# Kernel optimization log

Measured on AMD Instinct MI355X. Metric: run time of the kernel, lower is better.

The kernel has to match this reference:

```python
import jax, jax.numpy as jnp
import numpy as np

B, N, G, K, ENC = 8, 8192, 512, 32, 512
EPS = 1e-5


def setup_inputs() -> dict:
    key = jax.random.key(0)
    ks = jax.random.split(key, 8)
    def rn(k, shape, scale):
        return jax.random.normal(k, shape, dtype=jnp.float32) * scale
    return {
        "xyz": jax.random.normal(ks[0], (B, N, 3), dtype=jnp.float32),
        "color": jax.random.uniform(ks[1], (B, N, 3), dtype=jnp.float32),
        # Encoder.first_conv: Conv1d(6,128,1) -> LN(128) -> ReLU -> Conv1d(128,256,1)
        "w1": rn(ks[2], (128, 6), 0.4),   "b1": jnp.zeros((128,), jnp.float32),
        "g1": jnp.ones((128,), jnp.float32), "be1": jnp.zeros((128,), jnp.float32),
        "w2": rn(ks[3], (256, 128), 0.08), "b2": jnp.zeros((256,), jnp.float32),
        # Encoder.second_conv: Conv1d(512,512,1) -> LN(512) -> ReLU -> Conv1d(512,ENC,1)
        "w3": rn(ks[4], (512, 512), 0.04), "b3": jnp.zeros((512,), jnp.float32),
        "g2": jnp.ones((512,), jnp.float32), "be2": jnp.zeros((512,), jnp.float32),
        "w4": rn(ks[5], (ENC, 512), 0.04), "b4": jnp.zeros((ENC,), jnp.float32),
    }


def _fps_idx(xyz, num_samples):
    # Iterative farthest-point sampling, deterministic start at index 0 (pytorch3d default).
    b, n, _ = xyz.shape
    def body(carry, _):
        min_d, last = carry                                   # [B,N], [B]
        lp = jnp.take_along_axis(xyz, last[:, None, None], axis=1)  # [B,1,3]
        d = jnp.sum((xyz - lp) ** 2, axis=-1)                 # [B,N]
        min_d = jnp.minimum(min_d, d)
        nxt = jnp.argmax(min_d, axis=1).astype(jnp.int32)
        return (min_d, nxt), nxt
    init = (jnp.full((b, n), jnp.inf, dtype=xyz.dtype), jnp.zeros((b,), jnp.int32))
    _, rest = jax.lax.scan(body, init, None, length=num_samples - 1)
    return jnp.concatenate([jnp.zeros((1, b), jnp.int32), rest], axis=0).T  # [B,G]


def _layer_norm(x, g, b):
    mu = jnp.mean(x, axis=-1, keepdims=True)
    var = jnp.mean((x - mu) ** 2, axis=-1, keepdims=True)
    return (x - mu) * jax.lax.rsqrt(var + EPS) * g + b


def reference(xyz, color, w1, b1, g1, be1, w2, b2, w3, b3, g2, be2, w4, b4):
    # ---- Group: FPS centers + full pairwise sqdist + KNN top-k + gathers ----
    fidx = _fps_idx(xyz, G)                                   # [B,G]
    center = jax.vmap(lambda p, i: p[i])(xyz, fidx)           # [B,G,3]
    # square_distance(center, xyz) -> [B,G,N]
    d = (-2.0 * jnp.einsum('bgc,bnc->bgn', center, xyz)
         + jnp.sum(center ** 2, axis=-1)[:, :, None]
         + jnp.sum(xyz ** 2, axis=-1)[:, None, :])
    _, knn = jax.lax.top_k(-d, K)                             # [B,G,K] smallest distances
    gather = jax.vmap(lambda p, i: p[i])
    nbr_xyz = gather(xyz, knn.reshape(B, -1)).reshape(B, G, K, 3)
    nbr_col = gather(color, knn.reshape(B, -1)).reshape(B, G, K, 3)
    feats = jnp.concatenate([nbr_xyz - center[:, :, None, :], nbr_col], axis=-1)  # [B,G,K,6]
    # ---- Encoder: 1x1 convs == per-point linears (layer_norm variant) ----
    x = feats.reshape(B * G, K, 6)
    h = jnp.einsum('pkc,dc->pkd', x, w1) + b1                 # [BG,K,128]
    h = jax.nn.relu(_layer_norm(h, g1, be1))
    h = jnp.einsum('pkc,dc->pkd', h, w2) + b2                 # [BG,K,256]
    hg = jnp.max(h, axis=1, keepdims=True)                    # [BG,1,256] global max-pool
    h = jnp.concatenate([jnp.broadcast_to(hg, h.shape), h], axis=-1)  # [BG,K,512]
    h = jnp.einsum('pkc,dc->pkd', h, w3) + b3                 # [BG,K,512]
    h = jax.nn.relu(_layer_norm(h, g2, be2))
    h = jnp.einsum('pkc,dc->pkd', h, w4) + b4                 # [BG,K,ENC]
    return jnp.max(h, axis=1).reshape(B, G, ENC)
```

## Files before the change

### kernel.cpp

```cpp
#include <hip/hip_runtime.h>
#include <hip/hip_bf16.h>
#include <stdint.h>

constexpr int Bn = 8;
constexpr int Np = 8192;
constexpr int Gc = 512;
constexpr int Kn = 32;
constexpr int Mrows = Bn * Gc * Kn;
constexpr float LNEPS = 1e-5f;
constexpr int CNTS = 32;

using f32x2  = __attribute__((ext_vector_type(2))) float;
using f32x4  = __attribute__((ext_vector_type(4))) float;
using bf16x8 = __attribute__((ext_vector_type(8))) __bf16;

#define DEVINL __device__ __forceinline__

DEVINL unsigned wave_red_max_u32(unsigned x) {
    int v = (int)x, t;
    t = __builtin_amdgcn_update_dpp(0, v, 0x111, 0xf, 0xf, false); v = ((unsigned)v > (unsigned)t) ? v : t;
    t = __builtin_amdgcn_update_dpp(0, v, 0x112, 0xf, 0xf, false); v = ((unsigned)v > (unsigned)t) ? v : t;
    t = __builtin_amdgcn_update_dpp(0, v, 0x114, 0xf, 0xf, false); v = ((unsigned)v > (unsigned)t) ? v : t;
    t = __builtin_amdgcn_update_dpp(0, v, 0x118, 0xf, 0xf, false); v = ((unsigned)v > (unsigned)t) ? v : t;
    t = __builtin_amdgcn_update_dpp(0, v, 0x142, 0xa, 0xf, false); v = ((unsigned)v > (unsigned)t) ? v : t;
    t = __builtin_amdgcn_update_dpp(0, v, 0x143, 0xc, 0xf, false); v = ((unsigned)v > (unsigned)t) ? v : t;
    return (unsigned)__builtin_amdgcn_readlane(v, 63);
}
DEVINL unsigned wave_red_min_u32(unsigned x) {
    int v = (int)x, t;
    t = __builtin_amdgcn_update_dpp(-1, v, 0x111, 0xf, 0xf, false); v = ((unsigned)v < (unsigned)t) ? v : t;
    t = __builtin_amdgcn_update_dpp(-1, v, 0x112, 0xf, 0xf, false); v = ((unsigned)v < (unsigned)t) ? v : t;
    t = __builtin_amdgcn_update_dpp(-1, v, 0x114, 0xf, 0xf, false); v = ((unsigned)v < (unsigned)t) ? v : t;
    t = __builtin_amdgcn_update_dpp(-1, v, 0x118, 0xf, 0xf, false); v = ((unsigned)v < (unsigned)t) ? v : t;
    t = __builtin_amdgcn_update_dpp(-1, v, 0x142, 0xa, 0xf, false); v = ((unsigned)v < (unsigned)t) ? v : t;
    t = __builtin_amdgcn_update_dpp(-1, v, 0x143, 0xc, 0xf, false); v = ((unsigned)v < (unsigned)t) ? v : t;
    return (unsigned)__builtin_amdgcn_readlane(v, 63);
}
DEVINL unsigned long long wave_red_min_u64(unsigned long long x) {
    unsigned lo = (unsigned)x, hi = (unsigned)(x >> 32);
#define RSTEP(ctl, rm) { \
    unsigned tlo = (unsigned)__builtin_amdgcn_update_dpp(-1, (int)lo, ctl, rm, 0xf, false); \
    unsigned thi = (unsigned)__builtin_amdgcn_update_dpp(-1, (int)hi, ctl, rm, 0xf, false); \
    unsigned long long o = ((unsigned long long)thi << 32) | tlo; \
    unsigned long long c = ((unsigned long long)hi << 32) | lo; \
    if (o < c) { lo = tlo; hi = thi; } }
    RSTEP(0x111, 0xf) RSTEP(0x112, 0xf) RSTEP(0x114, 0xf) RSTEP(0x118, 0xf)
    RSTEP(0x142, 0xa) RSTEP(0x143, 0xc)
#undef RSTEP
    unsigned flo = (unsigned)__builtin_amdgcn_readlane((int)lo, 63);
    unsigned fhi = (unsigned)__builtin_amdgcn_readlane((int)hi, 63);
    return ((unsigned long long)fhi << 32) | flo;
}
DEVINL unsigned fkey(float f) {
    unsigned b = __float_as_uint(f);
    return b ^ (unsigned)(((int)b >> 31) | (int)0x80000000);
}

__global__ __launch_bounds__(512) void fps_knn_h1_kernel(
    const float* __restrict__ xyz, const float* __restrict__ color,
    const float* __restrict__ w1, const float* __restrict__ b1,
    const float* __restrict__ g1, const float* __restrict__ be1,
    __hip_bfloat16* __restrict__ h1b,
    unsigned* __restrict__ cnt, unsigned* __restrict__ cidx)
{
    alignas(16) __shared__ char shraw[131104];
    const int t = threadIdx.x;

    if (blockIdx.x < 8) {
        const int b = blockIdx.x;
        f32x4* pts = (f32x4*)shraw;
        unsigned long long* sred = (unsigned long long*)(shraw + 131072);
        const float* P = xyz + (size_t)b * Np * 3;
        f32x2 X[8], Y[8], Z[8], MD[8];
#pragma unroll
        for (int i = 0; i < 8; ++i) {
            int p0 = (2 * i) * 512 + t;
            int p1 = p0 + 512;
            float x0 = P[p0 * 3 + 0], y0 = P[p0 * 3 + 1], z0 = P[p0 * 3 + 2];
            float x1 = P[p1 * 3 + 0], y1 = P[p1 * 3 + 1], z1 = P[p1 * 3 + 2];
            X[i] = f32x2{x0, x1}; Y[i] = f32x2{y0, y1}; Z[i] = f32x2{z0, z1};
            pts[p0] = f32x4{x0, y0, z0, 0.f};
            pts[p1] = f32x4{x1, y1, z1, 0.f};
            MD[i] = f32x2{__builtin_inff(), __builtin_inff()};
        }
        if (t < 3) sred[t] = 0ull;
        if (t == 0) {
            __hip_atomic_store(&cidx[b * Gc + 0], 0u, __ATOMIC_RELAXED, __HIP_MEMORY_SCOPE_AGENT);
            __hip_atomic_store(&cnt[b * CNTS], 1u, __ATOMIC_RELEASE, __HIP_MEMORY_SCOPE_AGENT);
        }
        __syncthreads();
        int last = 0;
        for (int g = 1; g < Gc; ++g) {
            const f32x4 c4 = pts[last];
            const f32x2 cx = {c4.x, c4.x}, cy = {c4.y, c4.y}, cz = {c4.z, c4.z};
            f32x2 bv2 = {0.f, 0.f};
#pragma unroll
            for (int i = 0; i < 8; ++i) {
                f32x2 dx = X[i] - cx;
                f32x2 dy = Y[i] - cy;
                f32x2 dz = Z[i] - cz;
                f32x2 d  = (dx * dx + dy * dy) + dz * dz;
                f32x2 m  = MD[i];
                m.x = fminf(m.x, d.x); m.y = fminf(m.y, d.y);
                MD[i] = m;
                bv2.x = fmaxf(bv2.x, m.x); bv2.y = fmaxf(bv2.y, m.y);
            }
            const float bv = fmaxf(bv2.x, bv2.y);
            const unsigned wmax = wave_red_max_u32(__float_as_uint(bv));
            unsigned idx = 0xffffffffu;
#pragma unroll
            for (int i = 7; i >= 0; --i) {
                if (__float_as_uint(MD[i].y) == wmax) idx = (unsigned)((2 * i + 1) * 512 + t);
                if (__float_as_uint(MD[i].x) == wmax) idx = (unsigned)((2 * i) * 512 + t);
            }
            const unsigned widx = wave_red_min_u32(idx);
            if ((t & 63) == 0) {
                unsigned long long pack =
                    ((unsigned long long)wmax << 32) | (unsigned long long)(~widx);
                atomicMax(&sred[g % 3], pack);
            }
            if (t == 1) sred[(g + 1) % 3] = 0ull;
            __syncthreads();
            const unsigned long long w = sred[g % 3];
            const int wi = (int)(~(unsigned)w);
            if (t == 0) {
                __hip_atomic_store(&cidx[b * Gc + g], (unsigned)wi, __ATOMIC_RELAXED, __HIP_MEMORY_SCOPE_AGENT);
                if ((g & 7) == 7)
                    __hip_atomic_store(&cnt[b * CNTS], (unsigned)(g + 1), __ATOMIC_RELEASE, __HIP_MEMORY_SCOPE_AGENT);
            }
            last = wi;
        }
        return;
    }

    const int cid  = blockIdx.x - 8;
    const int cb   = cid & 7;
    const int cj   = cid >> 3;
    const int wave = t >> 6;
    const int sub  = wave & 3;
    const int gsel = wave >> 2;
    const int lane = t & 63;
    unsigned long long* wl = (unsigned long long*)shraw;
    float* fs = (float*)(shraw + 2048);
    const float* P = xyz + (size_t)cb * Np * 3;
    const float* C = color + (size_t)cb * Np * 3;
    const int pbase = sub * 2048 + lane;

    for (int p = cj; p < 256; p += 31) {
        const int g = 2 * p + gsel;
        if (t == 0) {
            while ((int)__hip_atomic_load(&cnt[cb * CNTS], __ATOMIC_ACQUIRE, __HIP_MEMORY_SCOPE_AGENT) < 2 * p + 2)
                __builtin_amdgcn_s_sleep(8);
        }
        __syncthreads();
        const unsigned wic = __hip_atomic_load(&cidx[cb * Gc + g], __ATOMIC_RELAXED, __HIP_MEMORY_SCOPE_AGENT);
        const float cx = P[wic * 3 + 0], cy = P[wic * 3 + 1], cz = P[wic * 3 + 2];
        const float cc = __fadd_rn(__fadd_rn(__fmul_rn(cx, cx), __fmul_rn(cy, cy)), __fmul_rn(cz, cz));
        float dr[32];
#pragma unroll
        for (int i = 0; i < 32; ++i) {
            int pp = pbase + i * 64;
            float px = P[pp * 3 + 0], py = P[pp * 3 + 1], pz = P[pp * 3 + 2];
            float dot = __fadd_rn(__fadd_rn(__fmul_rn(cx, px), __fmul_rn(cy, py)), __fmul_rn(cz, pz));
            float q   = __fadd_rn(__fadd_rn(__fmul_rn(px, px), __fmul_rn(py, py)), __fmul_rn(pz, pz));
            dr[i] = __fadd_rn(__fadd_rn(__fmul_rn(-2.0f, dot), cc), q);
        }
        unsigned excl = 0;
        for (int k = 0; k < Kn; ++k) {
            float bd = __builtin_inff();
            int   bs = 0;
#pragma unroll
            for (int i = 0; i < 32; ++i) {
                float d = ((excl >> i) & 1u) ? __builtin_inff() : dr[i];
                if (d < bd) { bd = d; bs = i; }
            }
            unsigned gidx = (unsigned)(pbase + bs * 64);
            unsigned long long win = wave_red_min_u64(
                ((unsigned long long)fkey(bd) << 32) | (unsigned long long)gidx);
            if (lane == 0) wl[gsel * 128 + sub * 32 + k] = win;
            unsigned widx = (unsigned)win;
            if ((widx & 63) == (unsigned)lane) excl |= 1u << ((widx >> 6) & 31);
        }
        __syncthreads();
        {
            const int tt = t & 255, half = t >> 8;
            if (tt < 128) {
                const unsigned long long my = wl[half * 128 + tt];
                int rank = 0;
                for (int j = 0; j < 128; ++j) rank += (wl[half * 128 + j] < my) ? 1 : 0;
                if (rank < Kn) {
                    unsigned gi = (unsigned)my;
                    float px = P[gi * 3 + 0], py = P[gi * 3 + 1], pz = P[gi * 3 + 2];
                    float* F = fs + (half * 32 + rank) * 6;
                    F[0] = px - cx; F[1] = py - cy; F[2] = pz - cz;
                    F[3] = C[gi * 3 + 0]; F[4] = C[gi * 3 + 1]; F[5] = C[gi * 3 + 2];
                }
            }
        }
        __syncthreads();
#pragma unroll
        for (int rr = 0; rr < 8; ++rr) {
            const int r  = wave * 8 + rr;
            const int gg = r >> 5, k = r & 31;
            const float* F = fs + (gg * 32 + k) * 6;
            float fr[6];
#pragma unroll
            for (int i = 0; i < 6; ++i) fr[i] = F[i];
            const int c0 = lane * 2;
            float a0 = b1[c0], a1 = b1[c0 + 1];
#pragma unroll
            for (int i = 0; i < 6; ++i) {
                a0 = fmaf(w1[c0 * 6 + i], fr[i], a0);
                a1 = fmaf(w1[(c0 + 1) * 6 + i], fr[i], a1);
            }
            float s = a0 + a1;
#pragma unroll
            for (int m = 1; m < 64; m <<= 1) s += __shfl_xor(s, m, 64);
            float mu = s * (1.f / 128.f);
            float d0 = a0 - mu, d1 = a1 - mu;
            float q = d0 * d0 + d1 * d1;
#pragma unroll
            for (int m = 1; m < 64; m <<= 1) q += __shfl_xor(q, m, 64);
            float iv = rsqrtf(q * (1.f / 128.f) + LNEPS);
            float y0 = fmaxf(0.f, d0 * iv * g1[c0] + be1[c0]);
            float y1 = fmaxf(0.f, d1 * iv * g1[c0 + 1] + be1[c0 + 1]);
            __hip_bfloat16* dst = h1b + ((size_t)(cb * Gc + 2 * p + gg) * 32 + k) * 128 + c0;
            dst[0] = __float2bfloat16(y0);
            dst[1] = __float2bfloat16(y1);
        }
        __syncthreads();
    }
}

__global__ void cast_w_kernel(const float* __restrict__ w2, const float* __restrict__ w3,
                              const float* __restrict__ w4,
                              __hip_bfloat16* __restrict__ o2, __hip_bfloat16* __restrict__ o3,
                              __hip_bfloat16* __restrict__ o4)
{
    int i = blockIdx.x * 256 + threadIdx.x;
    if (i < 256 * 128) o2[i] = __float2bfloat16(w2[i]);
    o3[i] = __float2bfloat16(w3[i]);
    o4[i] = __float2bfloat16(w4[i]);
}

template <int BN, int BK, int EPI>
__global__ __launch_bounds__(512, 2) void gemm_kernel(
    const __hip_bfloat16* A, int lda,
    const __hip_bfloat16* __restrict__ Bw, int ldb, int nkt,
    const float* __restrict__ bias,
    const float* __restrict__ gamma, const float* __restrict__ beta,
    __hip_bfloat16* outB, int ocol0,
    float* __restrict__ outF)
{
    constexpr int BM = 128;
    constexpr int WN = BN / 4;
    constexpr int NI = WN / 16;
    constexpr int MI = 4;
    constexpr int RB = BK * 2;
    constexpr int SWM = BK / 8 - 1;
    constexpr int A_ELE = BM * BK;
    constexpr int B_ELE = BN * BK;
    constexpr int BUF = A_ELE + B_ELE;
    constexpr int ACH = A_ELE * 2 / 16 / 512;
    constexpr int BCH = B_ELE * 2 / 16 / 512;
    __shared__ __hip_bfloat16 smem[2 * BUF];

    const int tid  = threadIdx.x;
    const int wid  = tid >> 6, lane = tid & 63;
    const int wm   = wid >> 2, wn = wid & 3;
    const int lrow = lane & 15, lq = lane >> 4;
    const int m0   = blockIdx.x * BM;

    f32x4 acc[MI][NI] = {};

    auto stage = [&](int buf, int k0) {
        const char* Ab = (const char*)A + ((size_t)m0 * lda + k0) * 2;
        const char* Bb = (const char*)Bw + (size_t)k0 * 2;
        char* sA = (char*)(smem + (size_t)buf * BUF);
        char* sB = sA + A_ELE * 2;
#pragma unroll
        for (int i = 0; i < ACH; ++i) {
            int chunk = i * 512 + tid;
            int Pp = chunk * 16;
            int row = Pp / RB;
            int kb = (Pp % RB) ^ ((row & SWM) << 4);
            const void* g = Ab + (size_t)row * (lda * 2) + kb;
            void* l = sA + (i * 512 + wid * 64) * 16;
            __builtin_amdgcn_global_load_lds((const __attribute__((address_space(1))) void*)g,
                                             (__attribute__((address_space(3))) void*)l, 16, 0, 0);
        }
#pragma unroll
        for (int i = 0; i < BCH; ++i) {
            int chunk = i * 512 + tid;
            int Pp = chunk * 16;
            int n = Pp / RB;
            int kb = (Pp % RB) ^ ((n & SWM) << 4);
            const void* g = Bb + (size_t)n * (ldb * 2) + kb;
            void* l = sB + (i * 512 + wid * 64) * 16;
            __builtin_amdgcn_global_load_lds((const __attribute__((address_space(1))) void*)g,
                                             (__attribute__((address_space(3))) void*)l, 16, 0, 0);
        }
    };

    auto compute = [&](int buf) {
        const char* sA = (const char*)(smem + (size_t)buf * BUF);
        const char* sB = sA + A_ELE * 2;
#pragma unroll
        for (int kk = 0; kk < BK / 32; ++kk) {
            bf16x8 af[MI], bfv[NI];
#pragma unroll
            for (int mi = 0; mi < MI; ++mi) {
                int row = wm * 64 + mi * 16 + lrow;
                int off = row * RB + ((kk * 64 + lq * 16) ^ ((row & SWM) << 4));
                af[mi] = *(const bf16x8*)(sA + off);
            }
#pragma unroll
            for (int ni = 0; ni < NI; ++ni) {
                int n = wn * WN + ni * 16 + lrow;
                int off = n * RB + ((kk * 64 + lq * 16) ^ ((n & SWM) << 4));
                bfv[ni] = *(const bf16x8*)(sB + off);
            }
#pragma unroll
            for (int mi = 0; mi < MI; ++mi)
#pragma unroll
                for (int ni = 0; ni < NI; ++ni)
                    acc[mi][ni] = __builtin_amdgcn_mfma_f32_16x16x32_bf16(af[mi], bfv[ni], acc[mi][ni], 0, 0, 0);
        }
    };

    stage(0, 0);
    __syncthreads();
    int cur = 0;
    for (int kt = 0; kt < nkt; ++kt) {
        if (kt + 1 < nkt) stage(cur ^ 1, (kt + 1) * BK);
        compute(cur);
        __syncthreads();
        cur ^= 1;
    }

    float bv[NI] = {};
    if constexpr (EPI != 6) {
#pragma unroll
        for (int ni = 0; ni < NI; ++ni) bv[ni] = bias[wn * WN + ni * 16 + lrow];
    }

    if constexpr (EPI == 5) {
#pragma unroll
        for (int mi = 0; mi < MI; ++mi)
#pragma unroll
            for (int ni = 0; ni < NI; ++ni) {
                int col = ocol0 + wn * WN + ni * 16 + lrow;
#pragma unroll
                for (int j = 0; j < 4; ++j) {
                    int row = wm * 64 + mi * 16 + lq * 4 + j;
                    outB[(size_t)(m0 + row) * 512 + col] = __float2bfloat16(acc[mi][ni][j] + bv[ni]);
                }
            }
        __hip_bfloat16* hgc = (__hip_bfloat16*)outF;
#pragma unroll
        for (int mi2 = 0; mi2 < 2; ++mi2) {
#pragma unroll
            for (int ni = 0; ni < NI; ++ni) {
                float m = -__builtin_inff();
#pragma unroll
                for (int mh = 0; mh < 2; ++mh) {
                    int mi = mi2 * 2 + mh;
#pragma unroll
                    for (int j = 0; j < 4; ++j) m = fmaxf(m, acc[mi][ni][j] + bv[ni]);
                }
                m = fmaxf(m, __shfl_xor(m, 16, 64));
                m = fmaxf(m, __shfl_xor(m, 32, 64));
                if (lq == 0) {
                    int grow = (m0 >> 5) + wm * 2 + mi2;
                    hgc[(size_t)grow * 256 + wn * WN + ni * 16 + lrow] = __float2bfloat16(m);
                }
            }
        }
    } else if constexpr (EPI == 4) {
#pragma unroll
        for (int mi = 0; mi < MI; ++mi)
#pragma unroll
            for (int ni = 0; ni < NI; ++ni) {
                int col = wn * WN + ni * 16 + lrow;
#pragma unroll
                for (int j = 0; j < 4; ++j) {
                    int row = wm * 64 + mi * 16 + lq * 4 + j;
                    outF[(size_t)(m0 + row) * 512 + col] = acc[mi][ni][j] + bv[ni];
                }
            }
    } else if constexpr (EPI == 6) {
        float gv[NI], bev[NI];
#pragma unroll
        for (int ni = 0; ni < NI; ++ni) {
            int col = wn * WN + ni * 16 + lrow;
            gv[ni] = gamma[col]; bev[ni] = beta[col];
        }
        {
            const float* P1 = outF;
#pragma unroll
            for (int mi = 0; mi < MI; ++mi) {
                int grow = (m0 >> 5) + wm * 2 + (mi >> 1);
#pragma unroll
                for (int ni = 0; ni < NI; ++ni) {
                    float ad = P1[(size_t)grow * 512 + (wn * WN + ni * 16 + lrow)];
#pragma unroll
                    for (int j = 0; j < 4; ++j) acc[mi][ni][j] += ad;
                }
            }
        }

        float* rs  = (float*)smem;
        float* rq  = rs + BM * 4;
        float* rmu = rq + BM * 4;
        float* riv = rmu + BM;
#pragma unroll
        for (int mi = 0; mi < MI; ++mi) {
#pragma unroll
            for (int j = 0; j < 4; ++j) {
                float s = 0.f, q = 0.f;
#pragma unroll
                for (int ni = 0; ni < NI; ++ni) { float v = acc[mi][ni][j]; s += v; q += v * v; }
#pragma unroll
                for (int m = 1; m < 16; m <<= 1) { s += __shfl_xor(s, m, 64); q += __shfl_xor(q, m, 64); }
                if (lrow == 0) {
                    int row = wm * 64 + mi * 16 + lq * 4 + j;
                    rs[row * 4 + wn] = s;
                    rq[row * 4 + wn] = q;
                }
            }
        }
        __syncthreads();
        if (tid < BM) {
            float S = rs[tid * 4 + 0] + rs[tid * 4 + 1] + rs[tid * 4 + 2] + rs[tid * 4 + 3];
            float Q = rq[tid * 4 + 0] + rq[tid * 4 + 1] + rq[tid * 4 + 2] + rq[tid * 4 + 3];
            float mu = S * (1.f / BN);
            float var = Q * (1.f / BN) - mu * mu;
            rmu[tid] = mu;
            riv[tid] = rsqrtf(var + LNEPS);
        }
        __syncthreads();
#pragma unroll
        for (int mi = 0; mi < MI; ++mi)
#pragma unroll
            for (int j = 0; j < 4; ++j) {
                int row = wm * 64 + mi * 16 + lq * 4 + j;
                float mu = rmu[row], iv = riv[row];
#pragma unroll
                for (int ni = 0; ni < NI; ++ni) {
                    float v = (acc[mi][ni][j] - mu) * iv * gv[ni] + bev[ni];
                    v = fmaxf(v, 0.f);
                    outB[(size_t)(m0 + row) * 512 + (wn * WN + ni * 16 + lrow)] = __float2bfloat16(v);
                }
            }
    } else {
#pragma unroll
        for (int grp = 0; grp < 2; ++grp) {
            float mx[NI];
#pragma unroll
            for (int ni = 0; ni < NI; ++ni) {
                float m = -__builtin_inff();
#pragma unroll
                for (int mh = 0; mh < 2; ++mh) {
                    int mi = grp * 2 + mh;
#pragma unroll
                    for (int j = 0; j < 4; ++j) m = fmaxf(m, acc[mi][ni][j] + bv[ni]);
                }
                mx[ni] = m;
            }
#pragma unroll
            for (int ni = 0; ni < NI; ++ni) {
                mx[ni] = fmaxf(mx[ni], __shfl_xor(mx[ni], 16, 64));
                mx[ni] = fmaxf(mx[ni], __shfl_xor(mx[ni], 32, 64));
            }
            if (lq == 0) {
                int grow = (m0 >> 5) + wm * 2 + grp;
#pragma unroll
                for (int ni = 0; ni < NI; ++ni)
                    outF[(size_t)grow * 512 + wn * WN + ni * 16 + lrow] = mx[ni];
            }
        }
    }
}

extern "C" void kernel_launch(void* const* d_in, const int* in_sizes, int n_in,
                              void* d_out, int out_size, void* d_ws, size_t ws_size,
                              hipStream_t stream)
{
    const float* xyz   = (const float*)d_in[0];
    const float* color = (const float*)d_in[1];
    const float* w1  = (const float*)d_in[2];
    const float* b1  = (const float*)d_in[3];
    const float* g1  = (const float*)d_in[4];
    const float* be1 = (const float*)d_in[5];
    const float* w2  = (const float*)d_in[6];
    const float* b2  = (const float*)d_in[7];
    const float* w3  = (const float*)d_in[8];
    const float* b3  = (const float*)d_in[9];
    const float* g2  = (const float*)d_in[10];
    const float* be2 = (const float*)d_in[11];
    const float* w4  = (const float*)d_in[12];
    const float* b4  = (const float*)d_in[13];
    float* out = (float*)d_out;

    char* ws = (char*)d_ws;
    size_t off = 0;
    auto alloc = [&](size_t bytes) -> void* {
        void* p = ws + off;
        off += (bytes + 255) & ~(size_t)255;
        return p;
    };
    unsigned* cnt       = (unsigned*)alloc((size_t)Bn * CNTS * 4);
    unsigned* cidx      = (unsigned*)alloc((size_t)Bn * Gc * 4);
    __hip_bfloat16* w2b = (__hip_bfloat16*)alloc((size_t)256 * 128 * 2);
    __hip_bfloat16* w3b = (__hip_bfloat16*)alloc((size_t)512 * 512 * 2);
    __hip_bfloat16* w4b = (__hip_bfloat16*)alloc((size_t)512 * 512 * 2);
    __hip_bfloat16* hgc = (__hip_bfloat16*)alloc((size_t)Bn * Gc * 256 * 2);
    __hip_bfloat16* h1b = (__hip_bfloat16*)alloc((size_t)Mrows * 128 * 2);
    __hip_bfloat16* x3  = (__hip_bfloat16*)alloc((size_t)Mrows * 512 * 2);
    float* P1 = (float*)h1b;
    (void)ws_size; (void)in_sizes; (void)n_in; (void)out_size;

    hipMemsetAsync(cnt, 0, (size_t)Bn * CNTS * 4, stream);
    fps_knn_h1_kernel<<<256, 512, 0, stream>>>(xyz, color, w1, b1, g1, be1, h1b, cnt, cidx);
    cast_w_kernel<<<1024, 256, 0, stream>>>(w2, w3, w4, w2b, w3b, w4b);
    gemm_kernel<256, 32, 5><<<Mrows / 128, 512, 0, stream>>>(h1b, 128, w2b, 128, 4,  b2, nullptr, nullptr, x3, 256, (float*)hgc);
    gemm_kernel<512, 32, 4><<<Bn * Gc / 128, 512, 0, stream>>>(hgc, 256, w3b, 512, 8, b3, nullptr, nullptr, nullptr, 0, P1);
    gemm_kernel<512, 32, 6><<<Mrows / 128, 512, 0, stream>>>(x3 + 256, 512, w3b + 256, 512, 8, nullptr, g2, be2, x3, 0, P1);
    gemm_kernel<512, 32, 2><<<Mrows / 128, 512, 0, stream>>>(x3, 512, w4b, 512, 16, b4, nullptr, nullptr, nullptr, 0, out);
}
```

Baseline: 653.3 us.

## Fuse whole encoder MLP into FPS/KNN consumer blocks with LDS-resident activations

Removes the four separate GEMM launches and global intermediates (h1, x3, hg, P1). Each consumer block now runs conv2, the global-feature matvec, conv3 with LayerNorm and conv4 with max-pool on its 64 rows, keeping activations in swizzled LDS. Weights are read straight from global or L2 without LDS staging. This trades large, well-tiled GEMMs for small 64-row MFMA tiles on only 248 blocks that overlap with FPS, so the encoder can now be hidden behind the serial FPS critical path. The risk is that the compute per block becomes the bottleneck.

Measured after the change: 1.621 ms. 2.48x slower.

```diff
diff --git a/kernel.cpp b/kernel.cpp
--- a/kernel.cpp
+++ b/kernel.cpp
@@ -6,7 +6,6 @@
 constexpr int Np = 8192;
 constexpr int Gc = 512;
 constexpr int Kn = 32;
-constexpr int Mrows = Bn * Gc * Kn;
 constexpr float LNEPS = 1e-5f;
 constexpr int CNTS = 32;
 
@@ -56,11 +55,28 @@
     return b ^ (unsigned)(((int)b >> 31) | (int)0x80000000);
 }
 
-__global__ __launch_bounds__(512) void fps_knn_h1_kernel(
+constexpr int WLOFF = 0;
+constexpr int FSOFF = 2048;
+constexpr int HGOFF = 3584;
+constexpr int P1OFF = 5632;
+constexpr int RSOFF = 9728;
+constexpr int RQOFF = 11776;
+constexpr int MUOFF = 13824;
+constexpr int IVOFF = 14080;
+constexpr int H1OFF = 14336;
+constexpr int H2OFF = 30720;
+constexpr int H3OFF = 63488;
+
+__global__ __launch_bounds__(512) void fused_net_kernel(
     const float* __restrict__ xyz, const float* __restrict__ color,
     const float* __restrict__ w1, const float* __restrict__ b1,
     const float* __restrict__ g1, const float* __restrict__ be1,
-    __hip_bfloat16* __restrict__ h1b,
+    const __hip_bfloat16* __restrict__ w2b, const __hip_bfloat16* __restrict__ w3b,
+    const __hip_bfloat16* __restrict__ w4b,
+    const float* __restrict__ b2, const float* __restrict__ b3,
+    const float* __restrict__ g2, const float* __restrict__ be2,
+    const float* __restrict__ b4,
+    float* __restrict__ out,
     unsigned* __restrict__ cnt, unsigned* __restrict__ cidx)
 {
     alignas(16) __shared__ char shraw[131104];
@@ -136,12 +152,19 @@
     const int cid  = blockIdx.x - 8;
     const int cb   = cid & 7;
     const int cj   = cid >> 3;
-    const int wave = t >> 6;
-    const int sub  = wave & 3;
-    const int gsel = wave >> 2;
+    const int wid  = t >> 6;
+    const int sub  = wid & 3;
+    const int gsel = wid >> 2;
     const int lane = t & 63;
-    unsigned long long* wl = (unsigned long long*)shraw;
-    float* fs = (float*)(shraw + 2048);
+    const int lrow = lane & 15, lq = lane >> 4;
+    unsigned long long* wl = (unsigned long long*)(shraw + WLOFF);
+    float* fs  = (float*)(shraw + FSOFF);
+    float* hgs = (float*)(shraw + HGOFF);
+    float* P1s = (float*)(shraw + P1OFF);
+    float* rs64 = (float*)(shraw + RSOFF);
+    float* rq64 = (float*)(shraw + RQOFF);
+    float* rmu = (float*)(shraw + MUOFF);
+    float* riv = (float*)(shraw + IVOFF);
     const float* P = xyz + (size_t)cb * Np * 3;
     const float* C = color + (size_t)cb * Np * 3;
     const int pbase = sub * 2048 + lane;
@@ -200,9 +223,8 @@
         __syncthreads();
 #pragma unroll
         for (int rr = 0; rr < 8; ++rr) {
-            const int r  = wave * 8 + rr;
-            const int gg = r >> 5, k = r & 31;
-            const float* F = fs + (gg * 32 + k) * 6;
+            const int r = wid * 8 + rr;
+            const float* F = fs + r * 6;
             float fr[6];
 #pragma unroll
             for (int i = 0; i < 6; ++i) fr[i] = F[i];
@@ -224,9 +246,196 @@
             float iv = rsqrtf(q * (1.f / 128.f) + LNEPS);
             float y0 = fmaxf(0.f, d0 * iv * g1[c0] + be1[c0]);
             float y1 = fmaxf(0.f, d1 * iv * g1[c0 + 1] + be1[c0 + 1]);
-            __hip_bfloat16* dst = h1b + ((size_t)(cb * Gc + 2 * p + gg) * 32 + k) * 128 + c0;
-            dst[0] = __float2bfloat16(y0);
-            dst[1] = __float2bfloat16(y1);
+            __hip_bfloat16 h0 = __float2bfloat16(y0), h1v = __float2bfloat16(y1);
+            unsigned pack = (unsigned)*(unsigned short*)&h0 | ((unsigned)*(unsigned short*)&h1v << 16);
+            *(unsigned*)(shraw + H1OFF + r * 256 + ((c0 * 2) ^ ((r & 15) << 4))) = pack;
+        }
+        __syncthreads();
+        {
+            const int n0 = wid * 32;
+            f32x4 a2[4][2] = {};
+#pragma unroll
+            for (int ks = 0; ks < 4; ++ks) {
+                bf16x8 af[4], bf2[2];
+#pragma unroll
+                for (int mi = 0; mi < 4; ++mi) {
+                    int row = mi * 16 + lrow;
+                    af[mi] = *(const bf16x8*)(shraw + H1OFF + row * 256 + ((ks * 64 + lq * 16) ^ ((row & 15) << 4)));
+                }
+#pragma unroll
+                for (int nt = 0; nt < 2; ++nt) {
+                    int n = n0 + nt * 16 + lrow;
+                    bf2[nt] = *(const bf16x8*)((const char*)w2b + (size_t)n * 256 + ks * 64 + lq * 16);
+                }
+#pragma unroll
+                for (int mi = 0; mi < 4; ++mi)
+#pragma unroll
+                    for (int nt = 0; nt < 2; ++nt)
+                        a2[mi][nt] = __builtin_amdgcn_mfma_f32_16x16x32_bf16(af[mi], bf2[nt], a2[mi][nt], 0, 0, 0);
+            }
+#pragma unroll
+            for (int nt = 0; nt < 2; ++nt) {
+                int col = n0 + nt * 16 + lrow;
+                float bb = b2[col];
+#pragma unroll
+                for (int mi = 0; mi < 4; ++mi)
+#pragma unroll
+                    for (int j = 0; j < 4; ++j) {
+                        float v = a2[mi][nt][j] + bb;
+                        a2[mi][nt][j] = v;
+                        int row = mi * 16 + lq * 4 + j;
+                        *(__hip_bfloat16*)(shraw + H2OFF + row * 512 + ((col * 2) ^ ((row & 31) << 4))) = __float2bfloat16(v);
+                    }
+#pragma unroll
+                for (int grp = 0; grp < 2; ++grp) {
+                    float m = -__builtin_inff();
+#pragma unroll
+                    for (int mh = 0; mh < 2; ++mh) {
+                        int mi = grp * 2 + mh;
+#pragma unroll
+                        for (int j = 0; j < 4; ++j) m = fmaxf(m, a2[mi][nt][j]);
+                    }
+                    m = fmaxf(m, __shfl_xor(m, 16, 64));
+                    m = fmaxf(m, __shfl_xor(m, 32, 64));
+                    if (lq == 0) hgs[grp * 256 + col] = m;
+                }
+            }
+        }
+        __syncthreads();
+        {
+            const int gg = t >> 8;
+            const int ob = t & 255;
+#pragma unroll
+            for (int half = 0; half < 2; ++half) {
+                int o = ob + half * 256;
+                float acc = b3[o];
+                const unsigned* wrow = (const unsigned*)((const char*)w3b + (size_t)o * 1024);
+#pragma unroll 8
+                for (int c = 0; c < 128; ++c) {
+                    unsigned u = wrow[c];
+                    float wlo = __uint_as_float(u << 16);
+                    float whi = __uint_as_float(u & 0xffff0000u);
+                    acc = fmaf(wlo, hgs[gg * 256 + 2 * c], acc);
+                    acc = fmaf(whi, hgs[gg * 256 + 2 * c + 1], acc);
+                }
+                P1s[gg * 512 + o] = acc;
+            }
+        }
+        __syncthreads();
+        {
+            const int n0 = wid * 64;
+            f32x4 a3[4][4] = {};
+#pragma unroll
+            for (int ks = 0; ks < 8; ++ks) {
+                bf16x8 af[4], bfv[4];
+#pragma unroll
+                for (int mi = 0; mi < 4; ++mi) {
+                    int row = mi * 16 + lrow;
+                    af[mi] = *(const bf16x8*)(shraw + H2OFF + row * 512 + ((ks * 64 + lq * 16) ^ ((row & 31) << 4)));
+                }
+#pragma unroll
+                for (int nt = 0; nt < 4; ++nt) {
+                    int n = n0 + nt * 16 + lrow;
+                    bfv[nt] = *(const bf16x8*)((const char*)w3b + (size_t)n * 1024 + 512 + ks * 64 + lq * 16);
+                }
+#pragma unroll
+                for (int mi = 0; mi < 4; ++mi)
+#pragma unroll
+                    for (int nt = 0; nt < 4; ++nt)
+                        a3[mi][nt] = __builtin_amdgcn_mfma_f32_16x16x32_bf16(af[mi], bfv[nt], a3[mi][nt], 0, 0, 0);
+            }
+#pragma unroll
+            for (int mi = 0; mi < 4; ++mi)
+#pragma unroll
+                for (int nt = 0; nt < 4; ++nt) {
+                    int col = n0 + nt * 16 + lrow;
+                    float ad = P1s[(mi >> 1) * 512 + col];
+#pragma unroll
+                    for (int j = 0; j < 4; ++j) a3[mi][nt][j] += ad;
+                }
+#pragma unroll
+            for (int mi = 0; mi < 4; ++mi)
+#pragma unroll
+                for (int j = 0; j < 4; ++j) {
+                    float s = 0.f, q = 0.f;
+#pragma unroll
+                    for (int nt = 0; nt < 4; ++nt) { float v = a3[mi][nt][j]; s += v; q += v * v; }
+#pragma unroll
+                    for (int m = 1; m < 16; m <<= 1) { s += __shfl_xor(s, m, 64); q += __shfl_xor(q, m, 64); }
+                    if (lrow == 0) {
+                        int row = mi * 16 + lq * 4 + j;
+                        rs64[row * 8 + wid] = s;
+                        rq64[row * 8 + wid] = q;
+                    }
+                }
+            __syncthreads();
+            if (t < 64) {
+                float S = 0.f, Q = 0.f;
+#pragma unroll
+                for (int w = 0; w < 8; ++w) { S += rs64[t * 8 + w]; Q += rq64[t * 8 + w]; }
+                float mu = S * (1.f / 512.f);
+                float var = Q * (1.f / 512.f) - mu * mu;
+                rmu[t] = mu;
+                riv[t] = rsqrtf(var + LNEPS);
+            }
+            __syncthreads();
+#pragma unroll
+            for (int mi = 0; mi < 4; ++mi)
+#pragma unroll
+                for (int j = 0; j < 4; ++j) {
+                    int row = mi * 16 + lq * 4 + j;
+                    float mu = rmu[row], iv = riv[row];
+#pragma unroll
+                    for (int nt = 0; nt < 4; ++nt) {
+                        int col = n0 + nt * 16 + lrow;
+                        float v = (a3[mi][nt][j] - mu) * iv * g2[col] + be2[col];
+                        v = fmaxf(v, 0.f);
+                        *(__hip_bfloat16*)(shraw + H3OFF + row * 1024 + ((col * 2) ^ ((row & 63) << 4))) = __float2bfloat16(v);
+                    }
+                }
+        }
+        __syncthreads();
+        {
+            const int n0 = wid * 64;
+            f32x4 a4[4][4] = {};
+#pragma unroll
+            for (int ks = 0; ks < 16; ++ks) {
+                bf16x8 af[4], bfv[4];
+#pragma unroll
+                for (int mi = 0; mi < 4; ++mi) {
+                    int row = mi * 16 + lrow;
+                    af[mi] = *(const bf16x8*)(shraw + H3OFF + row * 1024 + ((ks * 64 + lq * 16) ^ ((row & 63) << 4)));
+                }
+#pragma unroll
+                for (int nt = 0; nt < 4; ++nt) {
+                    int n = n0 + nt * 16 + lrow;
+                    bfv[nt] = *(const bf16x8*)((const char*)w4b + (size_t)n * 1024 + ks * 64 + lq * 16);
+                }
+#pragma unroll
+                for (int mi = 0; mi < 4; ++mi)
+#pragma unroll
+                    for (int nt = 0; nt < 4; ++nt)
+                        a4[mi][nt] = __builtin_amdgcn_mfma_f32_16x16x32_bf16(af[mi], bfv[nt], a4[mi][nt], 0, 0, 0);
+            }
+#pragma unroll
+            for (int nt = 0; nt < 4; ++nt) {
+                int col = n0 + nt * 16 + lrow;
+                float bb = b4[col];
+#pragma unroll
+                for (int grp = 0; grp < 2; ++grp) {
+                    float m = -__builtin_inff();
+#pragma unroll
+                    for (int mh = 0; mh < 2; ++mh) {
+                        int mi = grp * 2 + mh;
+#pragma unroll
+                        for (int j = 0; j < 4; ++j) m = fmaxf(m, a4[mi][nt][j] + bb);
+                    }
+                    m = fmaxf(m, __shfl_xor(m, 16, 64));
+                    m = fmaxf(m, __shfl_xor(m, 32, 64));
+                    if (lq == 0)
+                        out[(size_t)(cb * Gc + 2 * p + grp) * 512 + col] = m;
+                }
+            }
         }
         __syncthreads();
     }
@@ -241,245 +450,6 @@
     if (i < 256 * 128) o2[i] = __float2bfloat16(w2[i]);
     o3[i] = __float2bfloat16(w3[i]);
     o4[i] = __float2bfloat16(w4[i]);
-}
-
-template <int BN, int BK, int EPI>
-__global__ __launch_bounds__(512, 2) void gemm_kernel(
-    const __hip_bfloat16* A, int lda,
-    const __hip_bfloat16* __restrict__ Bw, int ldb, int nkt,
-    const float* __restrict__ bias,
-    const float* __restrict__ gamma, const float* __restrict__ beta,
-    __hip_bfloat16* outB, int ocol0,
-    float* __restrict__ outF)
-{
-    constexpr int BM = 128;
-    constexpr int WN = BN / 4;
-    constexpr int NI = WN / 16;
-    constexpr int MI = 4;
-    constexpr int RB = BK * 2;
-    constexpr int SWM = BK / 8 - 1;
-    constexpr int A_ELE = BM * BK;
-    constexpr int B_ELE = BN * BK;
-    constexpr int BUF = A_ELE + B_ELE;
-    constexpr int ACH = A_ELE * 2 / 16 / 512;
-    constexpr int BCH = B_ELE * 2 / 16 / 512;
-    __shared__ __hip_bfloat16 smem[2 * BUF];
-
-    const int tid  = threadIdx.x;
-    const int wid  = tid >> 6, lane = tid & 63;
-    const int wm   = wid >> 2, wn = wid & 3;
-    const int lrow = lane & 15, lq = lane >> 4;
-    const int m0   = blockIdx.x * BM;
-
-    f32x4 acc[MI][NI] = {};
-
-    auto stage = [&](int buf, int k0) {
-        const char* Ab = (const char*)A + ((size_t)m0 * lda + k0) * 2;
-        const char* Bb = (const char*)Bw + (size_t)k0 * 2;
-        char* sA = (char*)(smem + (size_t)buf * BUF);
-        char* sB = sA + A_ELE * 2;
-#pragma unroll
-        for (int i = 0; i < ACH; ++i) {
-            int chunk = i * 512 + tid;
-            int Pp = chunk * 16;
-            int row = Pp / RB;
-            int kb = (Pp % RB) ^ ((row & SWM) << 4);
-            const void* g = Ab + (size_t)row * (lda * 2) + kb;
-            void* l = sA + (i * 512 + wid * 64) * 16;
-            __builtin_amdgcn_global_load_lds((const __attribute__((address_space(1))) void*)g,
-                                             (__attribute__((address_space(3))) void*)l, 16, 0, 0);
-        }
-#pragma unroll
-        for (int i = 0; i < BCH; ++i) {
-            int chunk = i * 512 + tid;
-            int Pp = chunk * 16;
-            int n = Pp / RB;
-            int kb = (Pp % RB) ^ ((n & SWM) << 4);
-            const void* g = Bb + (size_t)n * (ldb * 2) + kb;
-            void* l = sB + (i * 512 + wid * 64) * 16;
-            __builtin_amdgcn_global_load_lds((const __attribute__((address_space(1))) void*)g,
-                                             (__attribute__((address_space(3))) void*)l, 16, 0, 0);
-        }
-    };
-
-    auto compute = [&](int buf) {
-        const char* sA = (const char*)(smem + (size_t)buf * BUF);
-        const char* sB = sA + A_ELE * 2;
-#pragma unroll
-        for (int kk = 0; kk < BK / 32; ++kk) {
-            bf16x8 af[MI], bfv[NI];
-#pragma unroll
-            for (int mi = 0; mi < MI; ++mi) {
-                int row = wm * 64 + mi * 16 + lrow;
-                int off = row * RB + ((kk * 64 + lq * 16) ^ ((row & SWM) << 4));
-                af[mi] = *(const bf16x8*)(sA + off);
-            }
-#pragma unroll
-            for (int ni = 0; ni < NI; ++ni) {
-                int n = wn * WN + ni * 16 + lrow;
-                int off = n * RB + ((kk * 64 + lq * 16) ^ ((n & SWM) << 4));
-                bfv[ni] = *(const bf16x8*)(sB + off);
-            }
-#pragma unroll
-            for (int mi = 0; mi < MI; ++mi)
-#pragma unroll
-                for (int ni = 0; ni < NI; ++ni)
-                    acc[mi][ni] = __builtin_amdgcn_mfma_f32_16x16x32_bf16(af[mi], bfv[ni], acc[mi][ni], 0, 0, 0);
-        }
-    };
-
-    stage(0, 0);
-    __syncthreads();
-    int cur = 0;
-    for (int kt = 0; kt < nkt; ++kt) {
-        if (kt + 1 < nkt) stage(cur ^ 1, (kt + 1) * BK);
-        compute(cur);
-        __syncthreads();
-        cur ^= 1;
-    }
-
-    float bv[NI] = {};
-    if constexpr (EPI != 6) {
-#pragma unroll
-        for (int ni = 0; ni < NI; ++ni) bv[ni] = bias[wn * WN + ni * 16 + lrow];
-    }
-
-    if constexpr (EPI == 5) {
-#pragma unroll
-        for (int mi = 0; mi < MI; ++mi)
-#pragma unroll
-            for (int ni = 0; ni < NI; ++ni) {
-                int col = ocol0 + wn * WN + ni * 16 + lrow;
-#pragma unroll
-                for (int j = 0; j < 4; ++j) {
-                    int row = wm * 64 + mi * 16 + lq * 4 + j;
-                    outB[(size_t)(m0 + row) * 512 + col] = __float2bfloat16(acc[mi][ni][j] + bv[ni]);
-                }
-            }
-        __hip_bfloat16* hgc = (__hip_bfloat16*)outF;
-#pragma unroll
-        for (int mi2 = 0; mi2 < 2; ++mi2) {
-#pragma unroll
-            for (int ni = 0; ni < NI; ++ni) {
-                float m = -__builtin_inff();
-#pragma unroll
-                for (int mh = 0; mh < 2; ++mh) {
-                    int mi = mi2 * 2 + mh;
-#pragma unroll
-                    for (int j = 0; j < 4; ++j) m = fmaxf(m, acc[mi][ni][j] + bv[ni]);
-                }
-                m = fmaxf(m, __shfl_xor(m, 16, 64));
-                m = fmaxf(m, __shfl_xor(m, 32, 64));
-                if (lq == 0) {
-                    int grow = (m0 >> 5) + wm * 2 + mi2;
-                    hgc[(size_t)grow * 256 + wn * WN + ni * 16 + lrow] = __float2bfloat16(m);
-                }
-            }
-        }
-    } else if constexpr (EPI == 4) {
-#pragma unroll
-        for (int mi = 0; mi < MI; ++mi)
-#pragma unroll
-            for (int ni = 0; ni < NI; ++ni) {
-                int col = wn * WN + ni * 16 + lrow;
-#pragma unroll
-                for (int j = 0; j < 4; ++j) {
-                    int row = wm * 64 + mi * 16 + lq * 4 + j;
-                    outF[(size_t)(m0 + row) * 512 + col] = acc[mi][ni][j] + bv[ni];
-                }
-            }
-    } else if constexpr (EPI == 6) {
-        float gv[NI], bev[NI];
-#pragma unroll
-        for (int ni = 0; ni < NI; ++ni) {
-            int col = wn * WN + ni * 16 + lrow;
-            gv[ni] = gamma[col]; bev[ni] = beta[col];
-        }
-        {
-            const float* P1 = outF;
-#pragma unroll
-            for (int mi = 0; mi < MI; ++mi) {
-                int grow = (m0 >> 5) + wm * 2 + (mi >> 1);
-#pragma unroll
-                for (int ni = 0; ni < NI; ++ni) {
-                    float ad = P1[(size_t)grow * 512 + (wn * WN + ni * 16 + lrow)];
-#pragma unroll
-                    for (int j = 0; j < 4; ++j) acc[mi][ni][j] += ad;
-                }
-            }
-        }
-
-        float* rs  = (float*)smem;
-        float* rq  = rs + BM * 4;
-        float* rmu = rq + BM * 4;
-        float* riv = rmu + BM;
-#pragma unroll
-        for (int mi = 0; mi < MI; ++mi) {
-#pragma unroll
-            for (int j = 0; j < 4; ++j) {
-                float s = 0.f, q = 0.f;
-#pragma unroll
-                for (int ni = 0; ni < NI; ++ni) { float v = acc[mi][ni][j]; s += v; q += v * v; }
-#pragma unroll
-                for (int m = 1; m < 16; m <<= 1) { s += __shfl_xor(s, m, 64); q += __shfl_xor(q, m, 64); }
-                if (lrow == 0) {
-                    int row = wm * 64 + mi * 16 + lq * 4 + j;
-                    rs[row * 4 + wn] = s;
-                    rq[row * 4 + wn] = q;
-                }
-            }
-        }
-        __syncthreads();
-        if (tid < BM) {
-            float S = rs[tid * 4 + 0] + rs[tid * 4 + 1] + rs[tid * 4 + 2] + rs[tid * 4 + 3];
-            float Q = rq[tid * 4 + 0] + rq[tid * 4 + 1] + rq[tid * 4 + 2] + rq[tid * 4 + 3];
-            float mu = S * (1.f / BN);
-            float var = Q * (1.f / BN) - mu * mu;
-            rmu[tid] = mu;
-            riv[tid] = rsqrtf(var + LNEPS);
-        }
-        __syncthreads();
-#pragma unroll
-        for (int mi = 0; mi < MI; ++mi)
-#pragma unroll
-            for (int j = 0; j < 4; ++j) {
-                int row = wm * 64 + mi * 16 + lq * 4 + j;
-                float mu = rmu[row], iv = riv[row];
-#pragma unroll
-                for (int ni = 0; ni < NI; ++ni) {
-                    float v = (acc[mi][ni][j] - mu) * iv * gv[ni] + bev[ni];
-                    v = fmaxf(v, 0.f);
-                    outB[(size_t)(m0 + row) * 512 + (wn * WN + ni * 16 + lrow)] = __float2bfloat16(v);
-                }
-            }
-    } else {
-#pragma unroll
-        for (int grp = 0; grp < 2; ++grp) {
-            float mx[NI];
-#pragma unroll
-            for (int ni = 0; ni < NI; ++ni) {
-                float m = -__builtin_inff();
-#pragma unroll
-                for (int mh = 0; mh < 2; ++mh) {
-                    int mi = grp * 2 + mh;
-#pragma unroll
-                    for (int j = 0; j < 4; ++j) m = fmaxf(m, acc[mi][ni][j] + bv[ni]);
-                }
-                mx[ni] = m;
-            }
-#pragma unroll
-            for (int ni = 0; ni < NI; ++ni) {
-                mx[ni] = fmaxf(mx[ni], __shfl_xor(mx[ni], 16, 64));
-                mx[ni] = fmaxf(mx[ni], __shfl_xor(mx[ni], 32, 64));
-            }
-            if (lq == 0) {
-                int grow = (m0 >> 5) + wm * 2 + grp;
-#pragma unroll
-                for (int ni = 0; ni < NI; ++ni)
-                    outF[(size_t)grow * 512 + wn * WN + ni * 16 + lrow] = mx[ni];
-            }
-        }
-    }
 }
 
 extern "C" void kernel_launch(void* const* d_in, const int* in_sizes, int n_in,
@@ -514,17 +484,11 @@
     __hip_bfloat16* w2b = (__hip_bfloat16*)alloc((size_t)256 * 128 * 2);
     __hip_bfloat16* w3b = (__hip_bfloat16*)alloc((size_t)512 * 512 * 2);
     __hip_bfloat16* w4b = (__hip_bfloat16*)alloc((size_t)512 * 512 * 2);
-    __hip_bfloat16* hgc = (__hip_bfloat16*)alloc((size_t)Bn * Gc * 256 * 2);
-    __hip_bfloat16* h1b = (__hip_bfloat16*)alloc((size_t)Mrows * 128 * 2);
-    __hip_bfloat16* x3  = (__hip_bfloat16*)alloc((size_t)Mrows * 512 * 2);
-    float* P1 = (float*)h1b;
     (void)ws_size; (void)in_sizes; (void)n_in; (void)out_size;
 
     hipMemsetAsync(cnt, 0, (size_t)Bn * CNTS * 4, stream);
-    fps_knn_h1_kernel<<<256, 512, 0, stream>>>(xyz, color, w1, b1, g1, be1, h1b, cnt, cidx);
     cast_w_kernel<<<1024, 256, 0, stream>>>(w2, w3, w4, w2b, w3b, w4b);
-    gemm_kernel<256, 32, 5><<<Mrows / 128, 512, 0, stream>>>(h1b, 128, w2b, 128, 4,  b2, nullptr, nullptr, x3, 256, (float*)hgc);
-    gemm_kernel<512, 32, 4><<<Bn * Gc / 128, 512, 0, stream>>>(hgc, 256, w3b, 512, 8, b3, nullptr, nullptr, nullptr, 0, P1);
-    gemm_kernel<512, 32, 6><<<Mrows / 128, 512, 0, stream>>>(x3 + 256, 512, w3b + 256, 512, 8, nullptr, g2, be2, x3, 0, P1);
-    gemm_kernel<512, 32, 2><<<Mrows / 128, 512, 0, stream>>>(x3, 512, w4b, 512, 16, b4, nullptr, nullptr, nullptr, 0, out);
-}
+    fused_net_kernel<<<256, 512, 0, stream>>>(xyz, color, w1, b1, g1, be1,
+                                              w2b, w3b, w4b, b2, b3, g2, be2, b4,
+                                              out, cnt, cidx);
+}
```
